# Kernel optimization log

Hardware: AMD Instinct MI355X
Metric: run time of the kernel (lower is better)

Reference implementation:

```python
import jax, jax.numpy as jnp
import numpy as np

B = 32          # number of graphs
N_PER = 1000    # num_nodes per graph (CDSQN.num_nodes)
TOTAL = B * N_PER
E = 512000      # edges (avg degree 16)
F_IN = 128      # node_feat_dim
HID = 128       # hidden_dim (= GNN embedding_dim)
D = 64          # dsf_hidden_dim
NH = 3          # num_heads
EPS = 1e-6


def setup_inputs() -> dict:
    key = jax.random.key(0)
    ks = jax.random.split(key, 12)
    x = jax.random.normal(ks[0], (TOTAL, F_IN), jnp.float32)
    edge_index = jax.random.randint(ks[1], (2, E), 0, TOTAL, dtype=jnp.int64)
    batch_index = jnp.repeat(jnp.arange(B, dtype=jnp.int64), N_PER)
    actions = (jax.random.uniform(ks[2], (B, N_PER)) < 0.1).astype(jnp.float32)

    def lin(k, fan_in, fan_out):
        s = 1.0 / np.sqrt(fan_in)
        return jax.random.uniform(k, (fan_in, fan_out), jnp.float32, -s, s)

    Wc1 = lin(ks[3], F_IN, HID); bc1 = jnp.zeros((HID,), jnp.float32)
    Wc2 = lin(ks[4], HID, HID);  bc2 = jnp.zeros((HID,), jnp.float32)
    Wc3 = lin(ks[5], HID, HID);  bc3 = jnp.zeros((HID,), jnp.float32)
    Wg1 = lin(ks[6], HID, NH * N_PER * D); bg1 = jnp.full((NH * N_PER * D,), 0.1, jnp.float32)
    Wg2 = lin(ks[7], HID, NH * D * D);     bg2 = jnp.full((NH * D * D,), 0.1, jnp.float32)
    Wg3 = lin(ks[8], HID, NH * D);         bg3 = jnp.full((NH * D,), 0.1, jnp.float32)
    return dict(x=x, edge_index=edge_index, batch_index=batch_index, actions=actions,
                Wc1=Wc1, bc1=bc1, Wc2=Wc2, bc2=bc2, Wc3=Wc3, bc3=bc3,
                Wg1=Wg1, bg1=bg1, Wg2=Wg2, bg2=bg2, Wg3=Wg3, bg3=bg3)


def _gcn(h, W, b, src, dst, norm):
    # PyG GCNConv: h' = D^-1/2 (A+I) D^-1/2 (h W) + b ; src/dst include self loops
    h = h @ W
    msgs = h[src] * norm[:, None]            # [E+TOTAL, out]
    return jax.ops.segment_sum(msgs, dst, num_segments=TOTAL) + b


def reference(x, edge_index, batch_index, actions,
              Wc1, bc1, Wc2, bc2, Wc3, bc3,
              Wg1, bg1, Wg2, bg2, Wg3, bg3):
    loops = jnp.arange(TOTAL, dtype=edge_index.dtype)
    src = jnp.concatenate([edge_index[0], loops])
    dst = jnp.concatenate([edge_index[1], loops])
    deg = jax.ops.segment_sum(jnp.ones(src.shape[0], x.dtype), dst, num_segments=TOTAL)
    dinv = jnp.where(deg > 0, jax.lax.rsqrt(deg), 0.0)
    norm = dinv[src] * dinv[dst]

    h = jax.nn.relu(_gcn(x, Wc1, bc1, src, dst, norm))
    h = jax.nn.relu(_gcn(h, Wc2, bc2, src, dst, norm))
    h = _gcn(h, Wc3, bc3, src, dst, norm)

    # global_mean_pool
    cnt = jax.ops.segment_sum(jnp.ones(TOTAL, x.dtype), batch_index, num_segments=B)
    h_g = jax.ops.segment_sum(h, batch_index, num_segments=B) / cnt[:, None]  # [B, HID]

    # hypernetwork weights
    w1 = jax.nn.softplus((h_g @ Wg1 + bg1).reshape(B, NH, N_PER, D))
    w2 = jax.nn.softplus((h_g @ Wg2 + bg2).reshape(B, NH, D, D))
    w3 = jax.nn.softplus((h_g @ Wg3 + bg3).reshape(B, NH, D))

    # compute_q (2D actions branch)
    h1 = jnp.einsum('bn,bhnd->bhd', actions, w1)
    h1 = jnp.sqrt(jnp.clip(h1, 0.0) + EPS)           # SafeSqrt
    h2 = jnp.einsum('bhd,bhde->bhe', h1, w2)
    h2 = jnp.log1p(jnp.clip(h2, 0.0))                # SafeLog: log(1+clamp(x,0))
    out_heads = jnp.einsum('bhd,bhd->bh', h2, w3)    # [B, NH]
    return jnp.min(out_heads, axis=-1)               # [B]
```

## Files before the change

### kernel.cpp

```cpp
#include <hip/hip_runtime.h>
#include <hip/hip_bf16.h>
#include <math.h>

#define NB 32
#define N_PER 1000
#define TOTALN 32000
#define NE 512000
#define HID 128
#define Dh 64
#define NH 3
#define EPSV 1e-6f
#define PCH 25
#define W1CH 250

typedef __attribute__((ext_vector_type(8))) short bf16x8;
typedef __attribute__((ext_vector_type(4))) float f32x4;

__device__ __forceinline__ float softplusf(float x) {
    return fmaxf(x, 0.0f) + log1pf(expf(-fabsf(x)));
}
__device__ __forceinline__ unsigned short f2b(float f) {
    __hip_bfloat16 h = __float2bfloat16(f);
    return __builtin_bit_cast(unsigned short, h);
}
__device__ __forceinline__ float b2f(unsigned short u) {
    unsigned int x = ((unsigned int)u) << 16;
    return __builtin_bit_cast(float, x);
}

__global__ __launch_bounds__(256) void k_init_deg(float* deg) {
    int i = blockIdx.x * 256 + threadIdx.x;
    if (i < TOTALN) deg[i] = 1.0f;
}

__global__ __launch_bounds__(256) void k_deg(const int* __restrict__ ei, float* deg) {
    int e = blockIdx.x * 256 + threadIdx.x;
    if (e < NE) atomicAdd(&deg[ei[NE + e]], 1.0f);
}

__global__ __launch_bounds__(256) void k_prep(float* __restrict__ d, int* __restrict__ cnt) {
    int i = blockIdx.x * 256 + threadIdx.x;
    if (i < TOTALN) {
        float v = d[i];
        cnt[i] = (int)v - 1;
        d[i] = rsqrtf(v);
    }
}

__global__ __launch_bounds__(256) void k_scan_block(const int* __restrict__ cnt,
                                                    int* __restrict__ rowptr,
                                                    int* __restrict__ bsum) {
    __shared__ int sh[256];
    int t = threadIdx.x;
    int i = blockIdx.x * 256 + t;
    int v = cnt[i];
    sh[t] = v;
    __syncthreads();
    for (int off = 1; off < 256; off <<= 1) {
        int add = (t >= off) ? sh[t - off] : 0;
        __syncthreads();
        sh[t] += add;
        __syncthreads();
    }
    rowptr[i] = sh[t] - v;
    if (t == 255) bsum[blockIdx.x] = sh[255];
}

__global__ void k_scan_tot(int* __restrict__ bsum) {
    if (threadIdx.x == 0) {
        int run = 0;
        for (int i = 0; i < 125; ++i) { int t = bsum[i]; bsum[i] = run; run += t; }
    }
}

__global__ __launch_bounds__(256) void k_scan_add(int* __restrict__ rowptr,
                                                  const int* __restrict__ bsum,
                                                  int* __restrict__ cursor) {
    int i = blockIdx.x * 256 + threadIdx.x;
    int v = rowptr[i] + bsum[blockIdx.x];
    rowptr[i] = v;
    cursor[i] = v;
    if (i == 0) rowptr[TOTALN] = NE;
}

__global__ __launch_bounds__(256) void k_fill(const int* __restrict__ ei,
                                              const float* __restrict__ dinv,
                                              int* __restrict__ cursor,
                                              int* __restrict__ csr_src,
                                              float* __restrict__ csr_w) {
    int e = blockIdx.x * 256 + threadIdx.x;
    if (e < NE) {
        int s = ei[e], d = ei[NE + e];
        int pos = atomicAdd(&cursor[d], 1);
        csr_src[pos] = s;
        csr_w[pos] = dinv[s] * dinv[d];
    }
}

__global__ __launch_bounds__(256) void k_wcvt3(const float* __restrict__ W1,
                                               const float* __restrict__ W2,
                                               const float* __restrict__ W3,
                                               unsigned short* __restrict__ Wt) {
    int i = blockIdx.x * 256 + threadIdx.x;
    int w = i >> 14, j = i & 16383;
    const float* W = (w == 0) ? W1 : (w == 1) ? W2 : W3;
    int k = j >> 7, c = j & 127;
    Wt[w * 16384 + c * 128 + k] = f2b(W[j]);
}

template<int INF32>
__global__ __launch_bounds__(256) void k_mm(const void* __restrict__ Xv,
                                            const unsigned short* __restrict__ Wt,
                                            unsigned short* __restrict__ Y) {
    int tid = threadIdx.x;
    int wv = tid >> 6, l = tid & 63;
    int row0 = blockIdx.x * 64 + wv * 16;
    int r = l & 15, kc = l >> 4;
    bf16x8 a[4];
    if (INF32) {
        const float* X = (const float*)Xv;
#pragma unroll
        for (int ks = 0; ks < 4; ++ks) {
            const float* p = X + (long)(row0 + r) * 128 + ks * 32 + kc * 8;
            float4 f0 = *(const float4*)p;
            float4 f1 = *(const float4*)(p + 4);
            bf16x8 t;
            t[0] = (short)f2b(f0.x); t[1] = (short)f2b(f0.y);
            t[2] = (short)f2b(f0.z); t[3] = (short)f2b(f0.w);
            t[4] = (short)f2b(f1.x); t[5] = (short)f2b(f1.y);
            t[6] = (short)f2b(f1.z); t[7] = (short)f2b(f1.w);
            a[ks] = t;
        }
    } else {
        const unsigned short* X = (const unsigned short*)Xv;
#pragma unroll
        for (int ks = 0; ks < 4; ++ks)
            a[ks] = *(const bf16x8*)(X + (long)(row0 + r) * 128 + ks * 32 + kc * 8);
    }
    f32x4 acc[8];
#pragma unroll
    for (int nt = 0; nt < 8; ++nt) acc[nt] = (f32x4){0.f, 0.f, 0.f, 0.f};
#pragma unroll
    for (int ks = 0; ks < 4; ++ks) {
#pragma unroll
        for (int nt = 0; nt < 8; ++nt) {
            bf16x8 b = *(const bf16x8*)(Wt + (nt * 16 + r) * 128 + ks * 32 + kc * 8);
            acc[nt] = __builtin_amdgcn_mfma_f32_16x16x32_bf16(a[ks], b, acc[nt], 0, 0, 0);
        }
    }
#pragma unroll
    for (int nt = 0; nt < 8; ++nt)
#pragma unroll
        for (int j = 0; j < 4; ++j)
            Y[(long)(row0 + kc * 4 + j) * 128 + nt * 16 + r] = f2b(acc[nt][j]);
}

template<int MODE>
__global__ __launch_bounds__(256) void k_gather(const unsigned short* __restrict__ feat,
                                                unsigned short* __restrict__ out,
                                                const int* __restrict__ rowptr,
                                                const int* __restrict__ csr_src,
                                                const float* __restrict__ csr_w,
                                                const float* __restrict__ dinv,
                                                const float* __restrict__ bias) {
    int wid = threadIdx.x >> 6, lane = threadIdx.x & 63;
    int v = blockIdx.x * 4 + wid;
    const unsigned int* f2 = (const unsigned int*)feat;
    float dv = dinv[v];
    unsigned int sv = f2[v * 64 + lane];
    float acc0 = b2f((unsigned short)(sv & 0xffff)) * dv * dv;
    float acc1 = b2f((unsigned short)(sv >> 16)) * dv * dv;
    int e = rowptr[v], e1 = rowptr[v + 1];
    for (; e + 4 <= e1; e += 4) {
        int s0 = csr_src[e], s1 = csr_src[e + 1], s2 = csr_src[e + 2], s3 = csr_src[e + 3];
        float w0 = csr_w[e], w1 = csr_w[e + 1], w2 = csr_w[e + 2], w3 = csr_w[e + 3];
        unsigned int u0 = f2[s0 * 64 + lane];
        unsigned int u1 = f2[s1 * 64 + lane];
        unsigned int u2 = f2[s2 * 64 + lane];
        unsigned int u3 = f2[s3 * 64 + lane];
        acc0 += b2f((unsigned short)(u0 & 0xffff)) * w0 + b2f((unsigned short)(u1 & 0xffff)) * w1
              + b2f((unsigned short)(u2 & 0xffff)) * w2 + b2f((unsigned short)(u3 & 0xffff)) * w3;
        acc1 += b2f((unsigned short)(u0 >> 16)) * w0 + b2f((unsigned short)(u1 >> 16)) * w1
              + b2f((unsigned short)(u2 >> 16)) * w2 + b2f((unsigned short)(u3 >> 16)) * w3;
    }
    for (; e < e1; ++e) {
        int s = csr_src[e];
        float w = csr_w[e];
        unsigned int u = f2[s * 64 + lane];
        acc0 += b2f((unsigned short)(u & 0xffff)) * w;
        acc1 += b2f((unsigned short)(u >> 16)) * w;
    }
    if (MODE == 0) {
        int c = lane * 2;
        acc0 = fmaxf(acc0 + bias[c], 0.f);
        acc1 = fmaxf(acc1 + bias[c + 1], 0.f);
    }
    ((unsigned int*)out)[v * 64 + lane] =
        (unsigned int)f2b(acc0) | ((unsigned int)f2b(acc1) << 16);
}

__global__ __launch_bounds__(256) void k_pool1(const unsigned short* __restrict__ A,
                                               float* __restrict__ pp) {
    __shared__ float sh[256];
    int b = blockIdx.x / PCH, ch = blockIdx.x % PCH;
    int c = threadIdx.x & 127, half = threadIdx.x >> 7;
    float acc = 0.f;
    int n0 = ch * 40;
#pragma unroll 4
    for (int j = half; j < 40; j += 2)
        acc += b2f(A[(long)(b * N_PER + n0 + j) * 128 + c]);
    sh[threadIdx.x] = acc;
    __syncthreads();
    if (threadIdx.x < 128)
        pp[blockIdx.x * 128 + c] = sh[c] + sh[128 + c];
}

__global__ __launch_bounds__(256) void k_pool2(const float* __restrict__ pp,
                                               const float* __restrict__ bias,
                                               float* __restrict__ hg,
                                               unsigned short* __restrict__ hgB) {
    int i = blockIdx.x * 256 + threadIdx.x;
    if (i >= NB * 128) return;
    int b = i >> 7, c = i & 127;
    float s = 0.f;
#pragma unroll
    for (int ch = 0; ch < PCH; ++ch)
        s += pp[(b * PCH + ch) * 128 + c];
    float v = s * (1.0f / N_PER) + bias[c];
    hg[i] = v;
    hgB[i] = f2b(v);
}

__global__ __launch_bounds__(256) void k_w1(const unsigned short* __restrict__ hgB,
                                            const float* __restrict__ Wg1,
                                            const float* __restrict__ bg1,
                                            const float* __restrict__ actions,
                                            float* __restrict__ p1) {
    __shared__ unsigned short wt[64][136];
    int h = blockIdx.x / W1CH, chunk = blockIdx.x % W1CH;
    int tid = threadIdx.x;
    int wv = tid >> 6, l = tid & 63;
    int r = l & 15, kc = l >> 4;
    const long KS = (long)NH * N_PER * Dh;
    bf16x8 a[2][4];
#pragma unroll
    for (int mt = 0; mt < 2; ++mt)
#pragma unroll
        for (int ks = 0; ks < 4; ++ks)
            a[mt][ks] = *(const bf16x8*)(hgB + (mt * 16 + r) * 128 + ks * 32 + kc * 8);
    float sp0[4] = {0.f, 0.f, 0.f, 0.f};
    float sp1[4] = {0.f, 0.f, 0.f, 0.f};
    int sd = tid & 63, sk = tid >> 6;
    for (int nn = 0; nn < 4; ++nn) {
        int n = chunk * 4 + nn;
        long colbase = (long)h * (N_PER * Dh) + (long)n * Dh;
        __syncthreads();
        const float* Wb = Wg1 + colbase + sd;
#pragma unroll 8
        for (int it = 0; it < 32; ++it) {
            int k = it * 4 + sk;
            wt[sd][k] = f2b(Wb[(long)k * KS]);
        }
        __syncthreads();
        f32x4 acc0 = (f32x4){0.f, 0.f, 0.f, 0.f};
        f32x4 acc1 = (f32x4){0.f, 0.f, 0.f, 0.f};
#pragma unroll
        for (int ks = 0; ks < 4; ++ks) {
            bf16x8 bb = *(const bf16x8*)&wt[wv * 16 + r][ks * 32 + kc * 8];
            acc0 = __builtin_amdgcn_mfma_f32_16x16x32_bf16(a[0][ks], bb, acc0, 0, 0, 0);
            acc1 = __builtin_amdgcn_mfma_f32_16x16x32_bf16(a[1][ks], bb, acc1, 0, 0, 0);
        }
        float bgv = bg1[colbase + wv * 16 + r];
#pragma unroll
        for (int j = 0; j < 4; ++j) {
            int b0 = kc * 4 + j;
            int b1 = 16 + kc * 4 + j;
            sp0[j] += softplusf(acc0[j] + bgv) * actions[b0 * N_PER + n];
            sp1[j] += softplusf(acc1[j] + bgv) * actions[b1 * N_PER + n];
        }
    }
    float* po = p1 + ((long)h * W1CH + chunk) * 2048;
#pragma unroll
    for (int j = 0; j < 4; ++j) {
        po[(kc * 4 + j) * 64 + wv * 16 + r] = sp0[j];
        po[(16 + kc * 4 + j) * 64 + wv * 16 + r] = sp1[j];
    }
}

__global__ __launch_bounds__(256) void k_red1(const float* __restrict__ p1,
                                              float* __restrict__ h1) {
    __shared__ float sh[4][64];
    int b = blockIdx.x / 3, h = blockIdx.x % 3;
    int part = threadIdx.x >> 6, d = threadIdx.x & 63;
    const float* base = p1 + (long)h * W1CH * 2048 + b * 64 + d;
    float s = 0.f;
    for (int ch = part; ch < W1CH; ch += 4)
        s += base[(long)ch * 2048];
    if (part) sh[part][d] = s;
    __syncthreads();
    if (part == 0)
        h1[(b * 3 + h) * 64 + d] = sqrtf(fmaxf(s + sh[1][d] + sh[2][d] + sh[3][d], 0.f) + EPSV);
}

__global__ __launch_bounds__(256) void k_w2(const float* __restrict__ hg,
                                            const float* __restrict__ Wg2,
                                            const float* __restrict__ bg2,
                                            const float* __restrict__ h1,
                                            float* __restrict__ p2) {
    __shared__ float hgs[32][128];
    __shared__ float wt[128][64];
    __shared__ float h1s[32];
    int hd = blockIdx.x;
    int tid = threadIdx.x;
    for (int i = 0; i < 16; ++i) {
        int idx = tid + i * 256;
        hgs[idx >> 7][idx & 127] = hg[idx];
    }
    long base = (long)hd * 64;
    for (int i = 0; i < 32; ++i) {
        int idx = tid + i * 256;
        wt[idx >> 6][idx & 63] = Wg2[(long)(idx >> 6) * (NH * Dh * Dh) + base + (idx & 63)];
    }
    int h = hd >> 6, d = hd & 63;
    if (tid < 32) h1s[tid] = h1[tid * (NH * Dh) + h * Dh + d];
    __syncthreads();
    int e = tid & 63, bq = tid >> 6;
    float bgv = bg2[base + e];
    float dot[8];
#pragma unroll
    for (int bi = 0; bi < 8; ++bi) dot[bi] = 0.f;
    for (int k = 0; k < 128; ++k) {
        float w = wt[k][e];
#pragma unroll
        for (int bi = 0; bi < 8; ++bi)
            dot[bi] += hgs[bq * 8 + bi][k] * w;
    }
    float* po = p2 + (long)hd * (32 * 64);
#pragma unroll
    for (int bi = 0; bi < 8; ++bi) {
        int b = bq * 8 + bi;
        po[b * 64 + e] = softplusf(dot[bi] + bgv) * h1s[b];
    }
}

__global__ __launch_bounds__(256) void k_red2(const float* __restrict__ p2,
                                              float* __restrict__ h2) {
    int o = blockIdx.x * 256 + threadIdx.x;
    if (o >= 32 * 192) return;
    int bh = o >> 6;
    int h = bh % 3, b = bh / 3;
    int e = o & 63;
    float s = 0.f;
    for (int d = 0; d < 64; ++d)
        s += p2[(h * 64 + d) * 2048 + b * 64 + e];
    h2[o] = log1pf(fmaxf(s, 0.f));
}

__global__ __launch_bounds__(192) void k_out(const float* __restrict__ hg,
                                             const float* __restrict__ Wg3,
                                             const float* __restrict__ bg3,
                                             const float* __restrict__ h2,
                                             float* __restrict__ out) {
    __shared__ float hgb[128];
    __shared__ float hres[NH];
    int b = blockIdx.x, tid = threadIdx.x;
    if (tid < 128) hgb[tid] = hg[b * 128 + tid];
    __syncthreads();
    int h = tid / 64, e = tid & 63;
    int c = h * 64 + e;
    float dot = 0.f;
    for (int k = 0; k < 128; ++k)
        dot += hgb[k] * Wg3[k * (NH * Dh) + c];
    float v = softplusf(dot + bg3[c]) * h2[b * 192 + c];
    for (int off = 32; off; off >>= 1)
        v += __shfl_down(v, off, 64);
    if (e == 0) hres[h] = v;
    __syncthreads();
    if (tid == 0) out[b] = fminf(fminf(hres[0], hres[1]), hres[2]);
}

extern "C" void kernel_launch(void* const* d_in, const int* in_sizes, int n_in,
                              void* d_out, int out_size, void* d_ws, size_t ws_size,
                              hipStream_t stream) {
    const float* x   = (const float*)d_in[0];
    const int*   ei  = (const int*)d_in[1];
    const float* act = (const float*)d_in[3];
    const float* Wc1 = (const float*)d_in[4];
    const float* bc1 = (const float*)d_in[5];
    const float* Wc2 = (const float*)d_in[6];
    const float* bc2 = (const float*)d_in[7];
    const float* Wc3 = (const float*)d_in[8];
    const float* bc3 = (const float*)d_in[9];
    const float* Wg1 = (const float*)d_in[10];
    const float* bg1 = (const float*)d_in[11];
    const float* Wg2 = (const float*)d_in[12];
    const float* bg2 = (const float*)d_in[13];
    const float* Wg3 = (const float*)d_in[14];
    const float* bg3 = (const float*)d_in[15];
    float* out = (float*)d_out;

    float* ws   = (float*)d_ws;
    float* dinv = ws;
    float* bufA = dinv + TOTALN;
    float* bufB = bufA + (long)TOTALN * 128;
    float* hg   = bufB + (long)TOTALN * 128;
    float* h1   = hg + 32 * 128;
    float* h2   = h1 + 32 * 192;
    float* csr_w = h2 + 32 * 192;
    float* pp   = csr_w + NE;
    unsigned short* hgB = (unsigned short*)(pp + NB * PCH * 128);
    int* cnt    = (int*)(hgB + 4096);
    int* rowptr = cnt + TOTALN;
    int* cursor = rowptr + TOTALN + 4;
    int* bsum   = cursor + TOTALN;
    int* csr_src= bsum + 128;
    unsigned short* Wt = (unsigned short*)(csr_src + NE);
    unsigned short* fA = (unsigned short*)bufA;
    unsigned short* fB = (unsigned short*)bufB;
    float* p1   = bufA;
    float* p2   = bufA + (long)NH * W1CH * 2048;

    k_init_deg<<<(TOTALN + 255) / 256, 256, 0, stream>>>(dinv);
    k_deg<<<NE / 256, 256, 0, stream>>>(ei, dinv);
    k_prep<<<(TOTALN + 255) / 256, 256, 0, stream>>>(dinv, cnt);
    k_scan_block<<<125, 256, 0, stream>>>(cnt, rowptr, bsum);
    k_scan_tot<<<1, 64, 0, stream>>>(bsum);
    k_scan_add<<<125, 256, 0, stream>>>(rowptr, bsum, cursor);
    k_fill<<<NE / 256, 256, 0, stream>>>(ei, dinv, cursor, csr_src, csr_w);
    k_wcvt3<<<192, 256, 0, stream>>>(Wc1, Wc2, Wc3, Wt);

    k_mm<1><<<500, 256, 0, stream>>>(x, Wt, fB);
    k_gather<0><<<TOTALN / 4, 256, 0, stream>>>(fB, fA, rowptr, csr_src, csr_w, dinv, bc1);
    k_mm<0><<<500, 256, 0, stream>>>(fA, Wt + 16384, fB);
    k_gather<0><<<TOTALN / 4, 256, 0, stream>>>(fB, fA, rowptr, csr_src, csr_w, dinv, bc2);
    k_mm<0><<<500, 256, 0, stream>>>(fA, Wt + 32768, fB);
    k_gather<1><<<TOTALN / 4, 256, 0, stream>>>(fB, fA, rowptr, csr_src, csr_w, dinv, nullptr);
    k_pool1<<<NB * PCH, 256, 0, stream>>>(fA, pp);
    k_pool2<<<(NB * 128 + 255) / 256, 256, 0, stream>>>(pp, bc3, hg, hgB);

    k_w1<<<NH * W1CH, 256, 0, stream>>>(hgB, Wg1, bg1, act, p1);
    k_red1<<<96, 256, 0, stream>>>(p1, h1);
    k_w2<<<NH * Dh, 256, 0, stream>>>(hg, Wg2, bg2, h1, p2);
    k_red2<<<24, 256, 0, stream>>>(p2, h2);
    k_out<<<NB, 192, 0, stream>>>(hg, Wg3, bg3, h2, out);
}
```

Measured before the change: 279.7 us.

## Fuse small kernels and restructure hypernetwork W1 stage with vectorized loads

Merges degree prep into the block scan, folds the global scan into the add kernel, and moves the h2 reduction into the output kernel, cutting several tiny launches. The W1 hypernetwork kernel now uses 1500 blocks handling two nodes each, loads Wg1 with float4 coalesced reads into a double-width LDS tile, and writes per-node products instead of accumulating in registers. The reduction is split across 8 segments per (batch, head) with atomics into a pre-zeroed buffer, and the sqrt is applied in k_w2. The p1 intermediate grows from 250 to 1000 node slices, which adds global write and read traffic in exchange for more parallelism and fewer launches.

```diff
diff --git a/kernel.cpp b/kernel.cpp
--- a/kernel.cpp
+++ b/kernel.cpp
@@ -11,7 +11,7 @@
 #define NH 3
 #define EPSV 1e-6f
 #define PCH 25
-#define W1CH 250
+#define W1CH 500
 
 typedef __attribute__((ext_vector_type(8))) short bf16x8;
 typedef __attribute__((ext_vector_type(4))) float f32x4;
@@ -28,9 +28,10 @@
     return __builtin_bit_cast(float, x);
 }
 
-__global__ __launch_bounds__(256) void k_init_deg(float* deg) {
+__global__ __launch_bounds__(256) void k_init(float* deg, float* h1pre) {
     int i = blockIdx.x * 256 + threadIdx.x;
     if (i < TOTALN) deg[i] = 1.0f;
+    if (i < 96 * 64) h1pre[i] = 0.f;
 }
 
 __global__ __launch_bounds__(256) void k_deg(const int* __restrict__ ei, float* deg) {
@@ -38,22 +39,15 @@
     if (e < NE) atomicAdd(&deg[ei[NE + e]], 1.0f);
 }
 
-__global__ __launch_bounds__(256) void k_prep(float* __restrict__ d, int* __restrict__ cnt) {
-    int i = blockIdx.x * 256 + threadIdx.x;
-    if (i < TOTALN) {
-        float v = d[i];
-        cnt[i] = (int)v - 1;
-        d[i] = rsqrtf(v);
-    }
-}
-
-__global__ __launch_bounds__(256) void k_scan_block(const int* __restrict__ cnt,
-                                                    int* __restrict__ rowptr,
-                                                    int* __restrict__ bsum) {
+__global__ __launch_bounds__(256) void k_scan1(float* __restrict__ deg,
+                                               int* __restrict__ rowptr,
+                                               int* __restrict__ bsum) {
     __shared__ int sh[256];
     int t = threadIdx.x;
     int i = blockIdx.x * 256 + t;
-    int v = cnt[i];
+    float dv = deg[i];
+    int v = (int)dv - 1;
+    deg[i] = rsqrtf(dv);
     sh[t] = v;
     __syncthreads();
     for (int off = 1; off < 256; off <<= 1) {
@@ -66,18 +60,22 @@
     if (t == 255) bsum[blockIdx.x] = sh[255];
 }
 
-__global__ void k_scan_tot(int* __restrict__ bsum) {
-    if (threadIdx.x == 0) {
+__global__ __launch_bounds__(256) void k_scan2(int* __restrict__ rowptr,
+                                               const int* __restrict__ bsum,
+                                               int* __restrict__ cursor) {
+    __shared__ int sh[128];
+    __shared__ int spre;
+    int t = threadIdx.x, bid = blockIdx.x;
+    if (t < 125) sh[t] = bsum[t];
+    __syncthreads();
+    if (t == 0) {
         int run = 0;
-        for (int i = 0; i < 125; ++i) { int t = bsum[i]; bsum[i] = run; run += t; }
-    }
-}
-
-__global__ __launch_bounds__(256) void k_scan_add(int* __restrict__ rowptr,
-                                                  const int* __restrict__ bsum,
-                                                  int* __restrict__ cursor) {
-    int i = blockIdx.x * 256 + threadIdx.x;
-    int v = rowptr[i] + bsum[blockIdx.x];
+        for (int j = 0; j < bid; ++j) run += sh[j];
+        spre = run;
+    }
+    __syncthreads();
+    int i = bid * 256 + t;
+    int v = rowptr[i] + spre;
     rowptr[i] = v;
     cursor[i] = v;
     if (i == 0) rowptr[TOTALN] = NE;
@@ -236,76 +234,76 @@
                                             const float* __restrict__ bg1,
                                             const float* __restrict__ actions,
                                             float* __restrict__ p1) {
-    __shared__ unsigned short wt[64][136];
+    __shared__ unsigned short wt[2][64][136];
     int h = blockIdx.x / W1CH, chunk = blockIdx.x % W1CH;
     int tid = threadIdx.x;
     int wv = tid >> 6, l = tid & 63;
     int r = l & 15, kc = l >> 4;
     const long KS = (long)NH * N_PER * Dh;
+    int n0 = chunk * 2;
+    long colbase2 = (long)h * (N_PER * Dh) + (long)n0 * Dh;
     bf16x8 a[2][4];
 #pragma unroll
     for (int mt = 0; mt < 2; ++mt)
 #pragma unroll
         for (int ks = 0; ks < 4; ++ks)
             a[mt][ks] = *(const bf16x8*)(hgB + (mt * 16 + r) * 128 + ks * 32 + kc * 8);
-    float sp0[4] = {0.f, 0.f, 0.f, 0.f};
-    float sp1[4] = {0.f, 0.f, 0.f, 0.f};
-    int sd = tid & 63, sk = tid >> 6;
-    for (int nn = 0; nn < 4; ++nn) {
-        int n = chunk * 4 + nn;
-        long colbase = (long)h * (N_PER * Dh) + (long)n * Dh;
-        __syncthreads();
-        const float* Wb = Wg1 + colbase + sd;
-#pragma unroll 8
-        for (int it = 0; it < 32; ++it) {
-            int k = it * 4 + sk;
-            wt[sd][k] = f2b(Wb[(long)k * KS]);
-        }
-        __syncthreads();
+    int kq = tid >> 5;
+    int j = (tid & 31) * 4;
+    int ns = j >> 6, ds = j & 63;
+#pragma unroll 4
+    for (int it = 0; it < 16; ++it) {
+        int k = it * 8 + kq;
+        float4 v = *(const float4*)(Wg1 + (long)k * KS + colbase2 + j);
+        wt[ns][ds][k]     = f2b(v.x);
+        wt[ns][ds + 1][k] = f2b(v.y);
+        wt[ns][ds + 2][k] = f2b(v.z);
+        wt[ns][ds + 3][k] = f2b(v.w);
+    }
+    __syncthreads();
+#pragma unroll
+    for (int nn = 0; nn < 2; ++nn) {
+        int n = n0 + nn;
         f32x4 acc0 = (f32x4){0.f, 0.f, 0.f, 0.f};
         f32x4 acc1 = (f32x4){0.f, 0.f, 0.f, 0.f};
 #pragma unroll
         for (int ks = 0; ks < 4; ++ks) {
-            bf16x8 bb = *(const bf16x8*)&wt[wv * 16 + r][ks * 32 + kc * 8];
+            bf16x8 bb = *(const bf16x8*)&wt[nn][wv * 16 + r][ks * 32 + kc * 8];
             acc0 = __builtin_amdgcn_mfma_f32_16x16x32_bf16(a[0][ks], bb, acc0, 0, 0, 0);
             acc1 = __builtin_amdgcn_mfma_f32_16x16x32_bf16(a[1][ks], bb, acc1, 0, 0, 0);
         }
-        float bgv = bg1[colbase + wv * 16 + r];
-#pragma unroll
-        for (int j = 0; j < 4; ++j) {
-            int b0 = kc * 4 + j;
-            int b1 = 16 + kc * 4 + j;
-            sp0[j] += softplusf(acc0[j] + bgv) * actions[b0 * N_PER + n];
-            sp1[j] += softplusf(acc1[j] + bgv) * actions[b1 * N_PER + n];
+        float bgv = bg1[colbase2 + nn * 64 + wv * 16 + r];
+        float* po = p1 + ((long)h * N_PER + n) * 2048;
+#pragma unroll
+        for (int jj = 0; jj < 4; ++jj) {
+            int b0 = kc * 4 + jj;
+            int b1 = 16 + kc * 4 + jj;
+            po[b0 * 64 + wv * 16 + r] = softplusf(acc0[jj] + bgv) * actions[b0 * N_PER + n];
+            po[b1 * 64 + wv * 16 + r] = softplusf(acc1[jj] + bgv) * actions[b1 * N_PER + n];
         }
     }
-    float* po = p1 + ((long)h * W1CH + chunk) * 2048;
-#pragma unroll
-    for (int j = 0; j < 4; ++j) {
-        po[(kc * 4 + j) * 64 + wv * 16 + r] = sp0[j];
-        po[(16 + kc * 4 + j) * 64 + wv * 16 + r] = sp1[j];
-    }
-}
-
-__global__ __launch_bounds__(256) void k_red1(const float* __restrict__ p1,
-                                              float* __restrict__ h1) {
+}
+
+__global__ __launch_bounds__(256) void k_red1a(const float* __restrict__ p1,
+                                               float* __restrict__ h1pre) {
     __shared__ float sh[4][64];
-    int b = blockIdx.x / 3, h = blockIdx.x % 3;
+    int bh = blockIdx.x >> 3, seg = blockIdx.x & 7;
+    int b = bh / 3, h = bh % 3;
     int part = threadIdx.x >> 6, d = threadIdx.x & 63;
-    const float* base = p1 + (long)h * W1CH * 2048 + b * 64 + d;
+    const float* base = p1 + (long)h * N_PER * 2048 + b * 64 + d;
     float s = 0.f;
-    for (int ch = part; ch < W1CH; ch += 4)
-        s += base[(long)ch * 2048];
+    for (int n = seg * 125 + part; n < seg * 125 + 125; n += 4)
+        s += base[(long)n * 2048];
     if (part) sh[part][d] = s;
     __syncthreads();
     if (part == 0)
-        h1[(b * 3 + h) * 64 + d] = sqrtf(fmaxf(s + sh[1][d] + sh[2][d] + sh[3][d], 0.f) + EPSV);
+        atomicAdd(&h1pre[bh * 64 + d], s + sh[1][d] + sh[2][d] + sh[3][d]);
 }
 
 __global__ __launch_bounds__(256) void k_w2(const float* __restrict__ hg,
                                             const float* __restrict__ Wg2,
                                             const float* __restrict__ bg2,
-                                            const float* __restrict__ h1,
+                                            const float* __restrict__ h1pre,
                                             float* __restrict__ p2) {
     __shared__ float hgs[32][128];
     __shared__ float wt[128][64];
@@ -322,7 +320,8 @@
         wt[idx >> 6][idx & 63] = Wg2[(long)(idx >> 6) * (NH * Dh * Dh) + base + (idx & 63)];
     }
     int h = hd >> 6, d = hd & 63;
-    if (tid < 32) h1s[tid] = h1[tid * (NH * Dh) + h * Dh + d];
+    if (tid < 32)
+        h1s[tid] = sqrtf(fmaxf(h1pre[(tid * 3 + h) * 64 + d], 0.f) + EPSV);
     __syncthreads();
     int e = tid & 63, bq = tid >> 6;
     float bgv = bg2[base + e];
@@ -343,23 +342,10 @@
     }
 }
 
-__global__ __launch_bounds__(256) void k_red2(const float* __restrict__ p2,
-                                              float* __restrict__ h2) {
-    int o = blockIdx.x * 256 + threadIdx.x;
-    if (o >= 32 * 192) return;
-    int bh = o >> 6;
-    int h = bh % 3, b = bh / 3;
-    int e = o & 63;
-    float s = 0.f;
-    for (int d = 0; d < 64; ++d)
-        s += p2[(h * 64 + d) * 2048 + b * 64 + e];
-    h2[o] = log1pf(fmaxf(s, 0.f));
-}
-
 __global__ __launch_bounds__(192) void k_out(const float* __restrict__ hg,
                                              const float* __restrict__ Wg3,
                                              const float* __restrict__ bg3,
-                                             const float* __restrict__ h2,
+                                             const float* __restrict__ p2,
                                              float* __restrict__ out) {
     __shared__ float hgb[128];
     __shared__ float hres[NH];
@@ -368,10 +354,15 @@
     __syncthreads();
     int h = tid / 64, e = tid & 63;
     int c = h * 64 + e;
+    float s = 0.f;
+#pragma unroll 8
+    for (int d = 0; d < 64; ++d)
+        s += p2[(long)(h * 64 + d) * 2048 + b * 64 + e];
+    float h2v = log1pf(fmaxf(s, 0.f));
     float dot = 0.f;
     for (int k = 0; k < 128; ++k)
         dot += hgb[k] * Wg3[k * (NH * Dh) + c];
-    float v = softplusf(dot + bg3[c]) * h2[b * 192 + c];
+    float v = softplusf(dot + bg3[c]) * h2v;
     for (int off = 32; off; off >>= 1)
         v += __shfl_down(v, off, 64);
     if (e == 0) hres[h] = v;
@@ -404,13 +395,11 @@
     float* bufA = dinv + TOTALN;
     float* bufB = bufA + (long)TOTALN * 128;
     float* hg   = bufB + (long)TOTALN * 128;
-    float* h1   = hg + 32 * 128;
-    float* h2   = h1 + 32 * 192;
-    float* csr_w = h2 + 32 * 192;
+    float* h1pre = hg + 32 * 128;
+    float* csr_w = h1pre + 96 * 64;
     float* pp   = csr_w + NE;
     unsigned short* hgB = (unsigned short*)(pp + NB * PCH * 128);
-    int* cnt    = (int*)(hgB + 4096);
-    int* rowptr = cnt + TOTALN;
+    int* rowptr = (int*)(hgB + 4096);
     int* cursor = rowptr + TOTALN + 4;
     int* bsum   = cursor + TOTALN;
     int* csr_src= bsum + 128;
@@ -418,14 +407,12 @@
     unsigned short* fA = (unsigned short*)bufA;
     unsigned short* fB = (unsigned short*)bufB;
     float* p1   = bufA;
-    float* p2   = bufA + (long)NH * W1CH * 2048;
-
-    k_init_deg<<<(TOTALN + 255) / 256, 256, 0, stream>>>(dinv);
+    float* p2   = bufA + (long)3 * N_PER * 2048;
+
+    k_init<<<(TOTALN + 255) / 256, 256, 0, stream>>>(dinv, h1pre);
     k_deg<<<NE / 256, 256, 0, stream>>>(ei, dinv);
-    k_prep<<<(TOTALN + 255) / 256, 256, 0, stream>>>(dinv, cnt);
-    k_scan_block<<<125, 256, 0, stream>>>(cnt, rowptr, bsum);
-    k_scan_tot<<<1, 64, 0, stream>>>(bsum);
-    k_scan_add<<<125, 256, 0, stream>>>(rowptr, bsum, cursor);
+    k_scan1<<<125, 256, 0, stream>>>(dinv, rowptr, bsum);
+    k_scan2<<<125, 256, 0, stream>>>(rowptr, bsum, cursor);
     k_fill<<<NE / 256, 256, 0, stream>>>(ei, dinv, cursor, csr_src, csr_w);
     k_wcvt3<<<192, 256, 0, stream>>>(Wc1, Wc2, Wc3, Wt);
 
@@ -439,8 +426,7 @@
     k_pool2<<<(NB * 128 + 255) / 256, 256, 0, stream>>>(pp, bc3, hg, hgB);
 
     k_w1<<<NH * W1CH, 256, 0, stream>>>(hgB, Wg1, bg1, act, p1);
-    k_red1<<<96, 256, 0, stream>>>(p1, h1);
-    k_w2<<<NH * Dh, 256, 0, stream>>>(hg, Wg2, bg2, h1, p2);
-    k_red2<<<24, 256, 0, stream>>>(p2, h2);
-    k_out<<<NB, 192, 0, stream>>>(hg, Wg3, bg3, h2, out);
-}
+    k_red1a<<<96 * 8, 256, 0, stream>>>(p1, h1pre);
+    k_w2<<<NH * Dh, 256, 0, stream>>>(hg, Wg2, bg2, h1pre, p2);
+    k_out<<<NB, 192, 0, stream>>>(hg, Wg3, bg3, p2, out);
+}
```

Result: faster. 267.1 us (-4.5%).
